# Performance work log

Measured on AMD Instinct MI355X. Metric: run time of the kernel, lower is better.

## Reference

```python
import jax, jax.numpy as jnp
import numpy as np

# Config (from Mamba3Config defaults)
D_MODEL = 768
EXPAND = 4
D_INNER = EXPAND * D_MODEL          # 3072
D_HEAD = 64
N_HEADS = D_INNER // D_HEAD         # 48
N_EXPERTS = 8
TOP_K = 2
R3 = 256                            # latent MoE input dim
R2 = 1024                           # latent MoE output dim
EPS = 1e-5
TANH_SCALE = 10.0                   # fast_scaled_tanh default
ROUTER_TEMP = 0.5                   # get_router_temperature(step=None) -> t_end


def _rms_norm(x, w):
    return x * jax.lax.rsqrt(jnp.mean(x * x, axis=-1, keepdims=True) + EPS) * w


def _scaled_tanh(x):
    return TANH_SCALE * jnp.tanh(x * (1.0 / TANH_SCALE))


def setup_inputs() -> dict:
    key = jax.random.key(0)
    ks = jax.random.split(key, 13)
    s = 0.02
    B, L = 2, 4096
    return {
        "x": jax.random.normal(ks[0], (B, L, D_MODEL), dtype=jnp.float32),
        "rms1_w": jnp.ones((D_MODEL,), jnp.float32),
        "W_in": s * jax.random.normal(ks[1], (D_MODEL, 2 * D_INNER + N_HEADS), jnp.float32),
        "dt_bias": jax.random.uniform(ks[2], (N_HEADS,), jnp.float32, -4.0, -1.0),  # dt in [dt_min, dt_max]-ish
        "W_out": s * jax.random.normal(ks[3], (D_INNER, D_MODEL), jnp.float32),
        "ls1": 0.01 * jnp.ones((D_MODEL,), jnp.float32),
        "rms2_w": jnp.ones((D_MODEL,), jnp.float32),
        "W_down": s * jax.random.normal(ks[4], (D_MODEL, R3), jnp.float32),
        "W_router": s * jax.random.normal(ks[5], (D_MODEL, N_EXPERTS), jnp.float32),
        "G": s * jax.random.normal(ks[6], (N_EXPERTS, R3, R2), jnp.float32),
        "W_up": s * jax.random.normal(ks[7], (R2, D_MODEL), jnp.float32),
        "ls2": 0.01 * jnp.ones((D_MODEL,), jnp.float32),
    }


def reference(x, rms1_w, W_in, dt_bias, W_out, ls1, rms2_w, W_down, W_router, G, W_up, ls2):
    B, L, _ = x.shape
    # ---- Mamba selective-scan branch ----
    xn = _rms_norm(x, rms1_w)
    proj = xn @ W_in                                   # [B,L,2*Di+H]
    u, z, dt = jnp.split(proj, [D_INNER, 2 * D_INNER], axis=-1)
    log_alpha = -jax.nn.softplus(dt + dt_bias)         # [B,L,H], per-head scalar decay
    alpha = jnp.exp(log_alpha)[..., None]              # [B,L,H,1]
    u4 = u.reshape(B, L, N_HEADS, D_HEAD)

    def combine(left, right):                          # first_order_combine_op
        a_l, b_l = left
        a_r, b_r = right
        return (a_r * a_l, a_r * b_l + b_r)

    _, h = jax.lax.associative_scan(
        combine, (jnp.broadcast_to(alpha, u4.shape), u4), axis=1)
    y = h.reshape(B, L, D_INNER) * jax.nn.silu(z)
    y = _scaled_tanh(y)
    x1 = x + ls1 * (y @ W_out)

    # ---- Fused latent MoE (Tucker) branch ----
    x2n = _rms_norm(x1, rms2_w)
    lat = _scaled_tanh(x2n @ W_down)                   # [B,L,r3]
    logits = (x2n @ W_router) * (1.0 / ROUTER_TEMP)    # [B,L,E]
    vals, idx = jax.lax.top_k(logits, TOP_K)
    probs = jax.nn.softmax(vals, axis=-1)              # [B,L,K]
    # dense combine weights: w[b,l,e] = sum_k probs_k * [idx_k == e]
    w = jnp.sum(jax.nn.one_hot(idx, N_EXPERTS, dtype=lat.dtype) * probs[..., None], axis=-2)
    # out[b,l,c] = sum_e w[b,l,e] * (lat[b,l,:] @ G[e])  (== fused gather grouped-GEMM)
    moe = jnp.einsum('blr,erc,ble->blc', lat, G, w)    # [B,L,r2]
    out = x1 + ls2 * (moe @ W_up)
    return out
```

## Files before the change

### kernel.cpp

```cpp
#include <hip/hip_runtime.h>
#include <stdint.h>

typedef unsigned short ushort_t;
typedef __attribute__((ext_vector_type(8))) __bf16 bf16x8;
typedef __attribute__((ext_vector_type(4))) float floatx4;
typedef __attribute__((ext_vector_type(4))) unsigned short ushort4v;
typedef __attribute__((ext_vector_type(8))) unsigned short ushort8v;

#define TT 8192L
#define LB 4096L
#define DD 768L
#define DI 3072L
#define NH 48L
#define R3C 256L
#define R2C 1024L
#define NP 6272L
#define CHS 64L

__device__ __forceinline__ float b2f(ushort_t u) {
  union { unsigned u32; float f; } v; v.u32 = ((unsigned)u) << 16; return v.f;
}
__device__ __forceinline__ ushort_t f2b(float f) {
  union { float f; unsigned u32; } v; v.f = f;
  unsigned r = v.u32 + 0x7FFFu + ((v.u32 >> 16) & 1u);
  return (ushort_t)(r >> 16);
}
__device__ __forceinline__ float fast_tanh(float x) {
  float e = __expf(2.0f * x);
  return 1.0f - 2.0f / (e + 1.0f);
}
__device__ __forceinline__ void g2l16(const void* g, void* l) {
  __builtin_amdgcn_global_load_lds(
      (const __attribute__((address_space(1))) unsigned int*)g,
      (__attribute__((address_space(3))) unsigned int*)l, 16, 0, 0);
}

__global__ __launch_bounds__(256) void k_tr_all(const float* __restrict__ s0, ushort_t* __restrict__ d0,
                                                const float* __restrict__ s1, ushort_t* __restrict__ d1,
                                                const float* __restrict__ s2, ushort_t* __restrict__ d2,
                                                const float* __restrict__ s3, ushort_t* __restrict__ d3,
                                                const float* __restrict__ s4, ushort_t* __restrict__ d4) {
  __shared__ float tile[64][65];
  int id = blockIdx.x;
  const float* src; ushort_t* dst; int K, N, gx;
  if (id < 1176)      {            src = s0; dst = d0; K = 768;  N = 6192; gx = 12; }
  else if (id < 1752) { id -= 1176; src = s1; dst = d1; K = 3072; N = 768;  gx = 48; }
  else if (id < 1800) { id -= 1752; src = s2; dst = d2; K = 768;  N = 256;  gx = 12; }
  else if (id < 1992) { id -= 1800; src = s3; dst = d3; K = 1024; N = 768;  gx = 16; }
  else                { id -= 1992; src = s4; dst = d4; K = 2048; N = 1024; gx = 32; }
  int k0 = (id % gx) * 64, n0 = (id / gx) * 64;
  int c = threadIdx.x & 63, r4 = threadIdx.x >> 6;
#pragma unroll
  for (int s = 0; s < 16; s++) {
    int r = s * 4 + r4;
    int n = n0 + c;
    tile[c][r] = (n < N) ? src[(long)(k0 + r) * N + n] : 0.0f;
  }
  __syncthreads();
#pragma unroll
  for (int s = 0; s < 16; s++) {
    int r = s * 4 + r4;
    dst[(long)(n0 + r) * K + k0 + c] = f2b(tile[r][c]);
  }
}

__global__ __launch_bounds__(256) void k_rms(const float* __restrict__ x,
                                             const float* __restrict__ w,
                                             ushort_t* __restrict__ out) {
  int t = blockIdx.x, tid = threadIdx.x;
  int lane = tid & 63, wid = tid >> 6;
  const float* xr = x + (long)t * DD;
  float v0 = xr[tid], v1 = xr[tid + 256], v2 = xr[tid + 512];
  float ss = v0 * v0 + v1 * v1 + v2 * v2;
  for (int o = 32; o; o >>= 1) ss += __shfl_down(ss, o);
  __shared__ float red[4];
  if (lane == 0) red[wid] = ss;
  __syncthreads();
  float tot = red[0] + red[1] + red[2] + red[3];
  float rr = rsqrtf(tot / 768.0f + 1e-5f);
  ushort_t* orow = out + (long)t * DD;
  orow[tid]       = f2b(v0 * rr * w[tid]);
  orow[tid + 256] = f2b(v1 * rr * w[tid + 256]);
  orow[tid + 512] = f2b(v2 * rr * w[tid + 512]);
}

__global__ __launch_bounds__(256) void k_fuse2(const float* __restrict__ P,
                                               const float* __restrict__ x,
                                               const float* __restrict__ ls1,
                                               const float* __restrict__ w2,
                                               const float* __restrict__ wr,
                                               ushort_t* __restrict__ x1,
                                               ushort_t* __restrict__ x2n,
                                               float* __restrict__ wrt) {
  int t = blockIdx.x, tid = threadIdx.x;
  int lane = tid & 63, wid = tid >> 6;
  int dd[3] = {tid, tid + 256, tid + 512};
  float v[3];
#pragma unroll
  for (int i = 0; i < 3; i++) {
    long ix = (long)t * DD + dd[i];
    float s = P[ix] + P[LB * DD + ix] + P[2 * LB * DD + ix] + P[3 * LB * DD + ix];
    float xv = x[ix] + ls1[dd[i]] * s;
    x1[ix] = f2b(xv);
    v[i] = xv;
  }
  float ss = v[0] * v[0] + v[1] * v[1] + v[2] * v[2];
  for (int o = 32; o; o >>= 1) ss += __shfl_down(ss, o);
  __shared__ float red[4];
  __shared__ float wred[4][8];
  __shared__ float slog[8];
  if (lane == 0) red[wid] = ss;
  __syncthreads();
  float tot = red[0] + red[1] + red[2] + red[3];
  float rr = rsqrtf(tot / 768.0f + 1e-5f);
  float p[8] = {0, 0, 0, 0, 0, 0, 0, 0};
  ushort_t* orow = x2n + (long)t * DD;
#pragma unroll
  for (int i = 0; i < 3; i++) {
    float xnv = v[i] * rr * w2[dd[i]];
    orow[dd[i]] = f2b(xnv);
    const float* wrow = wr + (long)dd[i] * 8;
#pragma unroll
    for (int e = 0; e < 8; e++) p[e] += xnv * wrow[e];
  }
#pragma unroll
  for (int e = 0; e < 8; e++) {
    float s = p[e];
    for (int o = 32; o; o >>= 1) s += __shfl_down(s, o);
    if (lane == 0) wred[wid][e] = s;
  }
  __syncthreads();
  if (tid < 8)
    slog[tid] = (wred[0][tid] + wred[1][tid] + wred[2][tid] + wred[3][tid]) * 2.0f;
  __syncthreads();
  if (tid == 0) {
    float l[8];
#pragma unroll
    for (int e = 0; e < 8; e++) l[e] = slog[e];
    int e0 = 0; float b0 = l[0];
#pragma unroll
    for (int e = 1; e < 8; e++) if (l[e] > b0) { b0 = l[e]; e0 = e; }
    int e1 = -1; float b1 = -1e30f;
#pragma unroll
    for (int e = 0; e < 8; e++) if (e != e0 && l[e] > b1) { b1 = l[e]; e1 = e; }
    float ex = __expf(b1 - b0);
    float pd = 1.0f / (1.0f + ex);
    float* wo = wrt + (long)t * 8;
#pragma unroll
    for (int e = 0; e < 8; e++) wo[e] = 0.0f;
    wo[e0] = pd;
    wo[e1] = ex * pd;
  }
}

__device__ __forceinline__ void stage_tile(const ushort_t* __restrict__ g, long rowstride,
                                           ushort_t* __restrict__ lds, int lane) {
  const int lrow = lane >> 3;
  const int dcol = (lane & 7) * 8;
#pragma unroll
  for (int c8 = 0; c8 < 8; c8++) {
    ushort8v v = *(const ushort8v*)(g + (long)(c8 * 8 + lrow) * rowstride + dcol);
    *(ushort8v*)&lds[(c8 * 64 + lane) * 8] = v;
  }
}

__device__ __forceinline__ float alpha_of(const ushort_t* __restrict__ proj, int tok, int h,
                                          const float* __restrict__ dtb) {
  float dt = b2f(proj[(long)tok * NP + 2 * DI + h]) + dtb[h];
  float sp = (dt > 20.0f) ? dt : log1pf(__expf(dt));
  return __expf(-sp);
}

__global__ __launch_bounds__(64) void k_scan1(const ushort_t* __restrict__ proj,
                                              const float* __restrict__ dtb,
                                              float* __restrict__ ssum,
                                              float* __restrict__ asum) {
  __shared__ __align__(16) ushort_t u_lds[64 * 64];
  __shared__ float s_alpha[64];
  const int lane = threadIdx.x;
  const int idx = blockIdx.x;
  const int c = idx & 63;
  const int h = idx >> 6;
  s_alpha[lane] = alpha_of(proj, (int)(c * CHS) + lane, h, dtb);
  const ushort_t* ug = proj + (long)c * CHS * NP + (long)h * 64;
  stage_tile(ug, NP, u_lds, lane);
  __syncthreads();
  float s = 0.0f, A = 1.0f;
#pragma unroll
  for (int tt = 0; tt < 64; tt++) {
    float a = s_alpha[tt];
    float u = b2f(u_lds[tt * 64 + lane]);
    s = fmaf(a, s, u);
    A *= a;
  }
  ssum[(long)idx * 64 + lane] = s;
  if (lane == 0) asum[idx] = A;
}

__global__ __launch_bounds__(64) void k_scan2(const float* __restrict__ ssum,
                                              const float* __restrict__ asum,
                                              float* __restrict__ carry) {
  int h = blockIdx.x, lane = threadIdx.x;
  float cv = 0.0f;
  for (int c = 0; c < 64; c++) {
    carry[((long)h * 64 + c) * 64 + lane] = cv;
    float A = asum[h * 64 + c];
    float s = ssum[((long)h * 64 + c) * 64 + lane];
    cv = A * cv + s;
  }
}

__global__ __launch_bounds__(64) void k_scan3(const ushort_t* __restrict__ proj,
                                              const float* __restrict__ dtb,
                                              const float* __restrict__ carry,
                                              ushort_t* __restrict__ y) {
  __shared__ __align__(16) ushort_t u_lds[64 * 64];
  __shared__ __align__(16) ushort_t z_lds[64 * 64];
  __shared__ float s_alpha[64];
  const int lane = threadIdx.x;
  const int idx = blockIdx.x;
  const int c = idx & 63;
  const int h = idx >> 6;
  s_alpha[lane] = alpha_of(proj, (int)(c * CHS) + lane, h, dtb);
  const ushort_t* ug = proj + (long)c * CHS * NP + (long)h * 64;
  const ushort_t* zg = ug + DI;
  ushort_t* yg = y + (long)c * CHS * DI + (long)h * 64;
  stage_tile(ug, NP, u_lds, lane);
  stage_tile(zg, NP, z_lds, lane);
  __syncthreads();
  float hs = carry[(long)idx * 64 + lane];
#pragma unroll
  for (int tt = 0; tt < 64; tt++) {
    float a = s_alpha[tt];
    float u = b2f(u_lds[tt * 64 + lane]);
    hs = fmaf(a, hs, u);
    float zv = b2f(z_lds[tt * 64 + lane]);
    float sig = 1.0f / (1.0f + __expf(-zv));
    float yv = hs * zv * sig;
    yv = 10.0f * fast_tanh(yv * 0.1f);
    yg[(long)tt * DI + lane] = f2b(yv);
  }
}

__global__ __launch_bounds__(256) void k_abig(const ushort_t* __restrict__ lat,
                                              const float* __restrict__ wrt,
                                              ushort_t* __restrict__ abig) {
  long gid = (long)blockIdx.x * 256 + threadIdx.x;
  long idx = gid * 4;
  int t = (int)(idx >> 11);
  int off = (int)(idx & 2047);
  int e = off >> 8, r = off & 255;
  float wv = wrt[(long)t * 8 + e];
  ushort4v lv = *(const ushort4v*)(lat + (long)t * R3C + r);
  ushort4v ov;
  ov.x = f2b(wv * b2f(lv.x));
  ov.y = f2b(wv * b2f(lv.y));
  ov.z = f2b(wv * b2f(lv.z));
  ov.w = f2b(wv * b2f(lv.w));
  *(ushort4v*)(abig + (long)t * 2048 + off) = ov;
}

template <int MODE>
__global__ __launch_bounds__(256, 4) void k_gemm(const ushort_t* __restrict__ A,
                                                 const ushort_t* __restrict__ Bt,
                                                 void* __restrict__ Cout, int K, int kstride,
                                                 int ldc, long zoff) {
  __shared__ __align__(16) ushort_t sA[2 * 128 * 32];
  __shared__ __align__(16) ushort_t sB[2 * 128 * 32];
  const int tid = threadIdx.x;
  const int lane = tid & 63, wid = tid >> 6;
  const int lm = lane & 15, q = lane >> 4;
  const int wm = wid >> 1, wn = wid & 1;
  const long row0 = (long)blockIdx.x * 128;
  const long col0 = (long)blockIdx.y * 128;
  const int z = blockIdx.z;
  A += (long)z * K;
  Bt += (long)z * K;

  floatx4 acc[4][4] = {};

  const int trow = tid >> 2;
  const int tcol = (tid & 3) * 8;
  const ushort_t* Ag = A + (row0 + trow) * (long)kstride + tcol;
  const ushort_t* Bg = Bt + (col0 + trow) * (long)kstride + tcol;
  const long rstep = 64L * kstride;

  for (int k0 = 0; k0 < K; k0 += 64) {
#pragma unroll
    for (int kk = 0; kk < 2; kk++)
#pragma unroll
      for (int rh = 0; rh < 2; rh++) {
        g2l16(Ag + rh * rstep + k0 + kk * 32, sA + kk * 4096 + rh * 2048 + wid * 512);
        g2l16(Bg + rh * rstep + k0 + kk * 32, sB + kk * 4096 + rh * 2048 + wid * 512);
      }
    __syncthreads();
#pragma unroll
    for (int kk = 0; kk < 2; kk++) {
      bf16x8 af[4], bfr[4];
#pragma unroll
      for (int i = 0; i < 4; i++)
        af[i] = *(const bf16x8*)(const void*)&sA[kk * 4096 + (wm * 64 + i * 16 + lm) * 32 + q * 8];
#pragma unroll
      for (int j = 0; j < 4; j++)
        bfr[j] = *(const bf16x8*)(const void*)&sB[kk * 4096 + (wn * 64 + j * 16 + lm) * 32 + q * 8];
#pragma unroll
      for (int i = 0; i < 4; i++)
#pragma unroll
        for (int j = 0; j < 4; j++)
          acc[i][j] = __builtin_amdgcn_mfma_f32_16x16x32_bf16(af[i], bfr[j], acc[i][j], 0, 0, 0);
    }
    __syncthreads();
  }
#pragma unroll
  for (int i = 0; i < 4; i++) {
#pragma unroll
    for (int r = 0; r < 4; r++) {
      long row = row0 + wm * 64 + i * 16 + q * 4 + r;
#pragma unroll
      for (int j = 0; j < 4; j++) {
        long col = col0 + wn * 64 + j * 16 + lm;
        float v = acc[i][j][r];
        if (MODE == 0) {
          ((ushort_t*)Cout)[row * (long)ldc + col] = f2b(v);
        } else {
          ((float*)Cout)[(long)z * zoff + row * (long)ldc + col] = v;
        }
      }
    }
  }
}

__global__ __launch_bounds__(256) void k_comb_tanh(const float* __restrict__ P, long zoff, int nz,
                                                   ushort_t* __restrict__ lat) {
  long i = ((long)blockIdx.x * 256 + threadIdx.x) * 4;
  float s[4] = {0, 0, 0, 0};
  for (int zz = 0; zz < nz; zz++) {
    const float* p = P + (long)zz * zoff + i;
#pragma unroll
    for (int j = 0; j < 4; j++) s[j] += p[j];
  }
#pragma unroll
  for (int j = 0; j < 4; j++) lat[i + j] = f2b(10.0f * fast_tanh(0.1f * s[j]));
}

__global__ __launch_bounds__(256) void k_comb_out(const float* __restrict__ P, long zoff, int nz,
                                                  const ushort_t* __restrict__ x1,
                                                  const float* __restrict__ ls,
                                                  float* __restrict__ outp) {
  long i = ((long)blockIdx.x * 256 + threadIdx.x) * 4;
  float s[4] = {0, 0, 0, 0};
  for (int zz = 0; zz < nz; zz++) {
    const float* p = P + (long)zz * zoff + i;
#pragma unroll
    for (int j = 0; j < 4; j++) s[j] += p[j];
  }
  int c = (int)(i % DD);
#pragma unroll
  for (int j = 0; j < 4; j++) outp[i + j] = b2f(x1[i + j]) + ls[c + j] * s[j];
}

#define OFF_WINT   0L
#define OFF_WOUTT  9633792L
#define OFF_WDNT   14352384L
#define OFF_WUPT   14745600L
#define OFF_GT     16318464L
#define OFF_X1     20512768L
#define OFF_WRT    33095680L
#define OFF_SSUM   34144256L
#define OFF_ASUM   34930688L
#define OFF_CARRY  34942976L
#define OFF_XN     35729408L
#define OFF_Y      48312320L
#define OFF_PROJ   73478144L
#define OFF_ABIG   OFF_PROJ
#define OFF_LAT    (OFF_PROJ + 33554432L)
#define OFF_PART   OFF_PROJ
#define OFF_X2N    OFF_XN
#define OFF_MOE    OFF_Y
#define WS_NEEDED  124858368L

extern "C" void kernel_launch(void* const* d_in, const int* in_sizes, int n_in,
                              void* d_out, int out_size, void* d_ws, size_t ws_size,
                              hipStream_t stream) {
  const float* x     = (const float*)d_in[0];
  const float* rms1w = (const float*)d_in[1];
  const float* W_in  = (const float*)d_in[2];
  const float* dtb   = (const float*)d_in[3];
  const float* W_out = (const float*)d_in[4];
  const float* ls1   = (const float*)d_in[5];
  const float* rms2w = (const float*)d_in[6];
  const float* W_dn  = (const float*)d_in[7];
  const float* W_rtr = (const float*)d_in[8];
  const float* G     = (const float*)d_in[9];
  const float* W_up  = (const float*)d_in[10];
  const float* ls2   = (const float*)d_in[11];
  if (ws_size < (size_t)WS_NEEDED) return;

  char* ws = (char*)d_ws;
  ushort_t* W_inT  = (ushort_t*)(ws + OFF_WINT);
  ushort_t* W_outT = (ushort_t*)(ws + OFF_WOUTT);
  ushort_t* W_dnT  = (ushort_t*)(ws + OFF_WDNT);
  ushort_t* W_upT  = (ushort_t*)(ws + OFF_WUPT);
  ushort_t* GT     = (ushort_t*)(ws + OFF_GT);
  ushort_t* x1     = (ushort_t*)(ws + OFF_X1);
  float*    wrt    = (float*)(ws + OFF_WRT);
  float*    ssum   = (float*)(ws + OFF_SSUM);
  float*    asum   = (float*)(ws + OFF_ASUM);
  float*    carry  = (float*)(ws + OFF_CARRY);
  ushort_t* xn     = (ushort_t*)(ws + OFF_XN);
  ushort_t* y      = (ushort_t*)(ws + OFF_Y);
  ushort_t* proj   = (ushort_t*)(ws + OFF_PROJ);
  ushort_t* abig   = (ushort_t*)(ws + OFF_ABIG);
  ushort_t* lat    = (ushort_t*)(ws + OFF_LAT);
  float*    part   = (float*)(ws + OFF_PART);
  ushort_t* x2n    = (ushort_t*)(ws + OFF_X2N);
  ushort_t* moe    = (ushort_t*)(ws + OFF_MOE);
  float*    outp   = (float*)d_out;

  k_tr_all<<<2504, 256, 0, stream>>>(W_in, W_inT, W_out, W_outT, W_dn, W_dnT,
                                     W_up, W_upT, G, GT);
  k_rms<<<8192, 256, 0, stream>>>(x, rms1w, xn);

  for (int b = 0; b < 2; b++) {
    const ushort_t* xnb = xn + (long)b * LB * DD;
    k_gemm<0><<<dim3(32, 49, 1), 256, 0, stream>>>(xnb, W_inT, proj, 768, 768, (int)NP, 0);
    k_scan1<<<3072, 64, 0, stream>>>(proj, dtb, ssum, asum);
    k_scan2<<<48, 64, 0, stream>>>(ssum, asum, carry);
    k_scan3<<<3072, 64, 0, stream>>>(proj, dtb, carry, y);
    k_gemm<4><<<dim3(32, 6, 4), 256, 0, stream>>>(y, W_outT, part, 768, 3072, 768, LB * DD);
    k_fuse2<<<4096, 256, 0, stream>>>(part, x + (long)b * LB * DD, ls1, rms2w, W_rtr,
                                      x1 + (long)b * LB * DD, x2n + (long)b * LB * DD,
                                      wrt + (long)b * LB * 8);
  }

  k_gemm<4><<<dim3(64, 2, 3), 256, 0, stream>>>(x2n, W_dnT, part, 256, 768, 256, TT * R3C);
  k_comb_tanh<<<2048, 256, 0, stream>>>(part, TT * R3C, 3, lat);
  k_abig<<<16384, 256, 0, stream>>>(lat, wrt, abig);
  k_gemm<0><<<dim3(64, 8, 1), 256, 0, stream>>>(abig, GT, moe, 2048, 2048, 1024, 0);
  k_gemm<4><<<dim3(64, 6, 2), 256, 0, stream>>>(moe, W_upT, part, 512, 1024, 768, TT * DD);
  k_comb_out<<<6144, 256, 0, stream>>>(part, TT * DD, 2, x1, ls2, outp);
}
```

Before: 519.0 us.

## Fuse prep kernels, inline scan carry, fuse MoE input, stage bf16 GEMM epilogue

Result: slower. 534.0 us (+2.9%).

```diff
diff --git a/kernel.cpp b/kernel.cpp
--- a/kernel.cpp
+++ b/kernel.cpp
@@ -4,7 +4,6 @@
 typedef unsigned short ushort_t;
 typedef __attribute__((ext_vector_type(8))) __bf16 bf16x8;
 typedef __attribute__((ext_vector_type(4))) float floatx4;
-typedef __attribute__((ext_vector_type(4))) unsigned short ushort4v;
 typedef __attribute__((ext_vector_type(8))) unsigned short ushort8v;
 
 #define TT 8192L
@@ -35,53 +34,54 @@
       (__attribute__((address_space(3))) unsigned int*)l, 16, 0, 0);
 }
 
-__global__ __launch_bounds__(256) void k_tr_all(const float* __restrict__ s0, ushort_t* __restrict__ d0,
-                                                const float* __restrict__ s1, ushort_t* __restrict__ d1,
-                                                const float* __restrict__ s2, ushort_t* __restrict__ d2,
-                                                const float* __restrict__ s3, ushort_t* __restrict__ d3,
-                                                const float* __restrict__ s4, ushort_t* __restrict__ d4) {
+__global__ __launch_bounds__(256) void k_prep(const float* __restrict__ s0, ushort_t* __restrict__ d0,
+                                              const float* __restrict__ s1, ushort_t* __restrict__ d1,
+                                              const float* __restrict__ s2, ushort_t* __restrict__ d2,
+                                              const float* __restrict__ s3, ushort_t* __restrict__ d3,
+                                              const float* __restrict__ s4, ushort_t* __restrict__ d4,
+                                              const float* __restrict__ x,
+                                              const float* __restrict__ w1,
+                                              ushort_t* __restrict__ xn) {
   __shared__ float tile[64][65];
   int id = blockIdx.x;
-  const float* src; ushort_t* dst; int K, N, gx;
-  if (id < 1176)      {            src = s0; dst = d0; K = 768;  N = 6192; gx = 12; }
-  else if (id < 1752) { id -= 1176; src = s1; dst = d1; K = 3072; N = 768;  gx = 48; }
-  else if (id < 1800) { id -= 1752; src = s2; dst = d2; K = 768;  N = 256;  gx = 12; }
-  else if (id < 1992) { id -= 1800; src = s3; dst = d3; K = 1024; N = 768;  gx = 16; }
-  else                { id -= 1992; src = s4; dst = d4; K = 2048; N = 1024; gx = 32; }
-  int k0 = (id % gx) * 64, n0 = (id / gx) * 64;
-  int c = threadIdx.x & 63, r4 = threadIdx.x >> 6;
-#pragma unroll
-  for (int s = 0; s < 16; s++) {
-    int r = s * 4 + r4;
-    int n = n0 + c;
-    tile[c][r] = (n < N) ? src[(long)(k0 + r) * N + n] : 0.0f;
-  }
-  __syncthreads();
-#pragma unroll
-  for (int s = 0; s < 16; s++) {
-    int r = s * 4 + r4;
-    dst[(long)(n0 + r) * K + k0 + c] = f2b(tile[r][c]);
-  }
-}
-
-__global__ __launch_bounds__(256) void k_rms(const float* __restrict__ x,
-                                             const float* __restrict__ w,
-                                             ushort_t* __restrict__ out) {
-  int t = blockIdx.x, tid = threadIdx.x;
-  int lane = tid & 63, wid = tid >> 6;
-  const float* xr = x + (long)t * DD;
-  float v0 = xr[tid], v1 = xr[tid + 256], v2 = xr[tid + 512];
-  float ss = v0 * v0 + v1 * v1 + v2 * v2;
-  for (int o = 32; o; o >>= 1) ss += __shfl_down(ss, o);
-  __shared__ float red[4];
-  if (lane == 0) red[wid] = ss;
-  __syncthreads();
-  float tot = red[0] + red[1] + red[2] + red[3];
-  float rr = rsqrtf(tot / 768.0f + 1e-5f);
-  ushort_t* orow = out + (long)t * DD;
-  orow[tid]       = f2b(v0 * rr * w[tid]);
-  orow[tid + 256] = f2b(v1 * rr * w[tid + 256]);
-  orow[tid + 512] = f2b(v2 * rr * w[tid + 512]);
+  if (id < 2504) {
+    const float* src; ushort_t* dst; int K, N, gx;
+    if (id < 1176)      {            src = s0; dst = d0; K = 768;  N = 6192; gx = 12; }
+    else if (id < 1752) { id -= 1176; src = s1; dst = d1; K = 3072; N = 768;  gx = 48; }
+    else if (id < 1800) { id -= 1752; src = s2; dst = d2; K = 768;  N = 256;  gx = 12; }
+    else if (id < 1992) { id -= 1800; src = s3; dst = d3; K = 1024; N = 768;  gx = 16; }
+    else                { id -= 1992; src = s4; dst = d4; K = 2048; N = 1024; gx = 32; }
+    int k0 = (id % gx) * 64, n0 = (id / gx) * 64;
+    int c = threadIdx.x & 63, r4 = threadIdx.x >> 6;
+#pragma unroll
+    for (int s = 0; s < 16; s++) {
+      int r = s * 4 + r4;
+      int n = n0 + c;
+      tile[c][r] = (n < N) ? src[(long)(k0 + r) * N + n] : 0.0f;
+    }
+    __syncthreads();
+#pragma unroll
+    for (int s = 0; s < 16; s++) {
+      int r = s * 4 + r4;
+      dst[(long)(n0 + r) * K + k0 + c] = f2b(tile[r][c]);
+    }
+  } else {
+    int t = id - 2504, tid = threadIdx.x;
+    int lane = tid & 63, wid = tid >> 6;
+    const float* xr = x + (long)t * DD;
+    float v0 = xr[tid], v1 = xr[tid + 256], v2 = xr[tid + 512];
+    float ss = v0 * v0 + v1 * v1 + v2 * v2;
+    for (int o = 32; o; o >>= 1) ss += __shfl_down(ss, o);
+    __shared__ float red[4];
+    if (lane == 0) red[wid] = ss;
+    __syncthreads();
+    float tot = red[0] + red[1] + red[2] + red[3];
+    float rr = rsqrtf(tot / 768.0f + 1e-5f);
+    ushort_t* orow = xn + (long)t * DD;
+    orow[tid]       = f2b(v0 * rr * w1[tid]);
+    orow[tid + 256] = f2b(v1 * rr * w1[tid + 256]);
+    orow[tid + 512] = f2b(v2 * rr * w1[tid + 512]);
+  }
 }
 
 __global__ __launch_bounds__(256) void k_fuse2(const float* __restrict__ P,
@@ -197,22 +197,10 @@
   if (lane == 0) asum[idx] = A;
 }
 
-__global__ __launch_bounds__(64) void k_scan2(const float* __restrict__ ssum,
-                                              const float* __restrict__ asum,
-                                              float* __restrict__ carry) {
-  int h = blockIdx.x, lane = threadIdx.x;
-  float cv = 0.0f;
-  for (int c = 0; c < 64; c++) {
-    carry[((long)h * 64 + c) * 64 + lane] = cv;
-    float A = asum[h * 64 + c];
-    float s = ssum[((long)h * 64 + c) * 64 + lane];
-    cv = A * cv + s;
-  }
-}
-
 __global__ __launch_bounds__(64) void k_scan3(const ushort_t* __restrict__ proj,
                                               const float* __restrict__ dtb,
-                                              const float* __restrict__ carry,
+                                              const float* __restrict__ ssum,
+                                              const float* __restrict__ asum,
                                               ushort_t* __restrict__ y) {
   __shared__ __align__(16) ushort_t u_lds[64 * 64];
   __shared__ __align__(16) ushort_t z_lds[64 * 64];
@@ -227,8 +215,13 @@
   ushort_t* yg = y + (long)c * CHS * DI + (long)h * 64;
   stage_tile(ug, NP, u_lds, lane);
   stage_tile(zg, NP, z_lds, lane);
-  __syncthreads();
-  float hs = carry[(long)idx * 64 + lane];
+  float hs = 0.0f;
+  for (int cc = 0; cc < c; cc++) {
+    float A = asum[h * 64 + cc];
+    float s = ssum[((long)(h * 64 + cc)) * 64 + lane];
+    hs = fmaf(A, hs, s);
+  }
+  __syncthreads();
 #pragma unroll
   for (int tt = 0; tt < 64; tt++) {
     float a = s_alpha[tt];
@@ -242,22 +235,19 @@
   }
 }
 
-__global__ __launch_bounds__(256) void k_abig(const ushort_t* __restrict__ lat,
-                                              const float* __restrict__ wrt,
-                                              ushort_t* __restrict__ abig) {
-  long gid = (long)blockIdx.x * 256 + threadIdx.x;
-  long idx = gid * 4;
-  int t = (int)(idx >> 11);
-  int off = (int)(idx & 2047);
-  int e = off >> 8, r = off & 255;
-  float wv = wrt[(long)t * 8 + e];
-  ushort4v lv = *(const ushort4v*)(lat + (long)t * R3C + r);
-  ushort4v ov;
-  ov.x = f2b(wv * b2f(lv.x));
-  ov.y = f2b(wv * b2f(lv.y));
-  ov.z = f2b(wv * b2f(lv.z));
-  ov.w = f2b(wv * b2f(lv.w));
-  *(ushort4v*)(abig + (long)t * 2048 + off) = ov;
+__global__ __launch_bounds__(256) void k_moe_in(const float* __restrict__ P,
+                                                const float* __restrict__ wrt,
+                                                ushort_t* __restrict__ abig) {
+  int t = blockIdx.x, d = threadIdx.x;
+  __shared__ float sw[8];
+  if (d < 8) sw[d] = wrt[(long)t * 8 + d];
+  long ix = (long)t * R3C + d;
+  float s = P[ix] + P[TT * R3C + ix] + P[2 * TT * R3C + ix];
+  __syncthreads();
+  float lv = 10.0f * fast_tanh(0.1f * s);
+  ushort_t* ab = abig + (long)t * 2048;
+#pragma unroll
+  for (int e = 0; e < 8; e++) ab[e * 256 + d] = f2b(sw[e] * lv);
 }
 
 template <int MODE>
@@ -311,36 +301,42 @@
     }
     __syncthreads();
   }
-#pragma unroll
-  for (int i = 0; i < 4; i++) {
-#pragma unroll
-    for (int r = 0; r < 4; r++) {
-      long row = row0 + wm * 64 + i * 16 + q * 4 + r;
-#pragma unroll
-      for (int j = 0; j < 4; j++) {
-        long col = col0 + wn * 64 + j * 16 + lm;
-        float v = acc[i][j][r];
-        if (MODE == 0) {
-          ((ushort_t*)Cout)[row * (long)ldc + col] = f2b(v);
-        } else {
-          ((float*)Cout)[(long)z * zoff + row * (long)ldc + col] = v;
+
+  if (MODE == 0) {
+    ushort_t* ep = ((wid & 2) ? sB : sA) + (wid & 1) * 2304;
+    ushort_t* Cb = (ushort_t*)Cout;
+    const int rr = lane >> 3, cc = (lane & 7) * 8;
+    __syncthreads();
+#pragma unroll
+    for (int p = 0; p < 2; p++) {
+#pragma unroll
+      for (int i2 = 0; i2 < 2; i2++)
+#pragma unroll
+        for (int j = 0; j < 4; j++)
+#pragma unroll
+          for (int r = 0; r < 4; r++)
+            ep[(i2 * 16 + q * 4 + r) * 72 + j * 16 + lm] = f2b(acc[p * 2 + i2][j][r]);
+#pragma unroll
+      for (int s = 0; s < 4; s++) {
+        ushort8v vv = *(const ushort8v*)&ep[(s * 8 + rr) * 72 + cc];
+        long grow = row0 + wm * 64 + p * 32 + s * 8 + rr;
+        *(ushort8v*)&Cb[grow * (long)ldc + col0 + wn * 64 + cc] = vv;
+      }
+    }
+  } else {
+#pragma unroll
+    for (int i = 0; i < 4; i++) {
+#pragma unroll
+      for (int r = 0; r < 4; r++) {
+        long row = row0 + wm * 64 + i * 16 + q * 4 + r;
+#pragma unroll
+        for (int j = 0; j < 4; j++) {
+          long col = col0 + wn * 64 + j * 16 + lm;
+          ((float*)Cout)[(long)z * zoff + row * (long)ldc + col] = acc[i][j][r];
         }
       }
     }
   }
-}
-
-__global__ __launch_bounds__(256) void k_comb_tanh(const float* __restrict__ P, long zoff, int nz,
-                                                   ushort_t* __restrict__ lat) {
-  long i = ((long)blockIdx.x * 256 + threadIdx.x) * 4;
-  float s[4] = {0, 0, 0, 0};
-  for (int zz = 0; zz < nz; zz++) {
-    const float* p = P + (long)zz * zoff + i;
-#pragma unroll
-    for (int j = 0; j < 4; j++) s[j] += p[j];
-  }
-#pragma unroll
-  for (int j = 0; j < 4; j++) lat[i + j] = f2b(10.0f * fast_tanh(0.1f * s[j]));
 }
 
 __global__ __launch_bounds__(256) void k_comb_out(const float* __restrict__ P, long zoff, int nz,
@@ -368,15 +364,15 @@
 #define OFF_WRT    33095680L
 #define OFF_SSUM   34144256L
 #define OFF_ASUM   34930688L
-#define OFF_CARRY  34942976L
 #define OFF_XN     35729408L
 #define OFF_Y      48312320L
 #define OFF_PROJ   73478144L
+#define OFF_X2N    OFF_XN
+#define OFF_PART   OFF_PROJ
+#define OFF_DPART  OFF_Y
 #define OFF_ABIG   OFF_PROJ
-#define OFF_LAT    (OFF_PROJ + 33554432L)
-#define OFF_PART   OFF_PROJ
-#define OFF_X2N    OFF_XN
 #define OFF_MOE    OFF_Y
+#define OFF_UPART  OFF_PROJ
 #define WS_NEEDED  124858368L
 
 extern "C" void kernel_launch(void* const* d_in, const int* in_sizes, int n_in,
@@ -406,37 +402,34 @@
   float*    wrt    = (float*)(ws + OFF_WRT);
   float*    ssum   = (float*)(ws + OFF_SSUM);
   float*    asum   = (float*)(ws + OFF_ASUM);
-  float*    carry  = (float*)(ws + OFF_CARRY);
   ushort_t* xn     = (ushort_t*)(ws + OFF_XN);
   ushort_t* y      = (ushort_t*)(ws + OFF_Y);
   ushort_t* proj   = (ushort_t*)(ws + OFF_PROJ);
+  float*    part   = (float*)(ws + OFF_PART);
+  float*    dpart  = (float*)(ws + OFF_DPART);
   ushort_t* abig   = (ushort_t*)(ws + OFF_ABIG);
-  ushort_t* lat    = (ushort_t*)(ws + OFF_LAT);
-  float*    part   = (float*)(ws + OFF_PART);
+  ushort_t* moe    = (ushort_t*)(ws + OFF_MOE);
+  float*    upart  = (float*)(ws + OFF_UPART);
   ushort_t* x2n    = (ushort_t*)(ws + OFF_X2N);
-  ushort_t* moe    = (ushort_t*)(ws + OFF_MOE);
   float*    outp   = (float*)d_out;
 
-  k_tr_all<<<2504, 256, 0, stream>>>(W_in, W_inT, W_out, W_outT, W_dn, W_dnT,
-                                     W_up, W_upT, G, GT);
-  k_rms<<<8192, 256, 0, stream>>>(x, rms1w, xn);
+  k_prep<<<10696, 256, 0, stream>>>(W_in, W_inT, W_out, W_outT, W_dn, W_dnT,
+                                    W_up, W_upT, G, GT, x, rms1w, xn);
 
   for (int b = 0; b < 2; b++) {
     const ushort_t* xnb = xn + (long)b * LB * DD;
     k_gemm<0><<<dim3(32, 49, 1), 256, 0, stream>>>(xnb, W_inT, proj, 768, 768, (int)NP, 0);
     k_scan1<<<3072, 64, 0, stream>>>(proj, dtb, ssum, asum);
-    k_scan2<<<48, 64, 0, stream>>>(ssum, asum, carry);
-    k_scan3<<<3072, 64, 0, stream>>>(proj, dtb, carry, y);
+    k_scan3<<<3072, 64, 0, stream>>>(proj, dtb, ssum, asum, y);
     k_gemm<4><<<dim3(32, 6, 4), 256, 0, stream>>>(y, W_outT, part, 768, 3072, 768, LB * DD);
     k_fuse2<<<4096, 256, 0, stream>>>(part, x + (long)b * LB * DD, ls1, rms2w, W_rtr,
                                       x1 + (long)b * LB * DD, x2n + (long)b * LB * DD,
                                       wrt + (long)b * LB * 8);
   }
 
-  k_gemm<4><<<dim3(64, 2, 3), 256, 0, stream>>>(x2n, W_dnT, part, 256, 768, 256, TT * R3C);
-  k_comb_tanh<<<2048, 256, 0, stream>>>(part, TT * R3C, 3, lat);
-  k_abig<<<16384, 256, 0, stream>>>(lat, wrt, abig);
+  k_gemm<4><<<dim3(64, 2, 3), 256, 0, stream>>>(x2n, W_dnT, dpart, 256, 768, 256, TT * R3C);
+  k_moe_in<<<8192, 256, 0, stream>>>(dpart, wrt, abig);
   k_gemm<0><<<dim3(64, 8, 1), 256, 0, stream>>>(abig, GT, moe, 2048, 2048, 1024, 0);
-  k_gemm<4><<<dim3(64, 6, 2), 256, 0, stream>>>(moe, W_upT, part, 512, 1024, 768, TT * DD);
-  k_comb_out<<<6144, 256, 0, stream>>>(part, TT * DD, 2, x1, ls2, outp);
-}
+  k_gemm<4><<<dim3(64, 6, 2), 256, 0, stream>>>(moe, W_upT, upart, 512, 1024, 768, TT * DD);
+  k_comb_out<<<6144, 256, 0, stream>>>(upart, TT * DD, 2, x1, ls2, outp);
+}
```
